# Optimization experiments

Measured on AMD Instinct MI355X. Metric: run time of the kernel, lower is better.

Reference implementation:

```python
import jax, jax.numpy as jnp
import numpy as np

D_MODEL = 1024
N_HEADS = 16
SEQ = 4096
BATCH = 1
THETA = 10000.0


def setup_inputs() -> dict:
    key = jax.random.key(0)
    ks = jax.random.split(key, 5)
    std = np.sqrt(2.0 / (D_MODEL + D_MODEL))
    x = jax.random.normal(ks[0], (BATCH, SEQ, D_MODEL), dtype=jnp.float32)
    Wq = jax.random.normal(ks[1], (D_MODEL, D_MODEL), dtype=jnp.float32) * std
    Wk = jax.random.normal(ks[2], (D_MODEL, D_MODEL), dtype=jnp.float32) * std
    Wv = jax.random.normal(ks[3], (D_MODEL, D_MODEL), dtype=jnp.float32) * std
    Wo = jax.random.normal(ks[4], (D_MODEL, D_MODEL), dtype=jnp.float32) * std
    token_positions = jnp.arange(SEQ, dtype=jnp.int32)
    return {"x": x, "Wq": Wq, "Wk": Wk, "Wv": Wv, "Wo": Wo,
            "token_positions": token_positions}


def _rope(x, positions):
    # x: [b, h, s, d]; positions: [s]
    d = x.shape[-1]
    ks = jnp.arange(0, d, 2, dtype=jnp.float32)
    inv_freq = 1.0 / jnp.power(jnp.float32(THETA), ks / d)          # [d/2]
    ang = positions.astype(jnp.float32)[:, None] * inv_freq[None, :]  # [s, d/2]
    cos, sin = jnp.cos(ang), jnp.sin(ang)
    x_even, x_odd = x[..., 0::2], x[..., 1::2]
    y_even = cos * x_even - sin * x_odd
    y_odd = sin * x_even + cos * x_odd
    # interleave back: [..., d/2, 2] -> [..., d]
    return jnp.stack([y_even, y_odd], axis=-1).reshape(x.shape)


def reference(x, Wq, Wk, Wv, Wo, token_positions):
    b, s, _ = x.shape
    h = N_HEADS
    d = D_MODEL // h

    def proj(W):
        y = jnp.einsum('bsi,oi->bso', x, W)
        return y.reshape(b, s, h, d).transpose(0, 2, 1, 3)  # [b,h,s,d]

    Q, K, V = proj(Wq), proj(Wk), proj(Wv)
    Q = _rope(Q, token_positions)
    K = _rope(K, token_positions)

    scale = 1.0 / np.sqrt(d)
    scores = jnp.einsum('bhqd,bhkd->bhqk', Q, K) * scale  # [b,h,s,s]
    causal = jnp.tril(jnp.ones((s, s), dtype=bool))
    scores = jnp.where(causal, scores, -jnp.inf)
    attn = jax.nn.softmax(scores, axis=-1)
    ctx = jnp.einsum('bhqk,bhkd->bhqd', attn, V)
    ctx = ctx.transpose(0, 2, 1, 3).reshape(b, s, D_MODEL)
    return jnp.einsum('bsi,oi->bso', ctx, Wo)
```

## Files before the change

### kernel.cpp

```cpp
#include <hip/hip_runtime.h>
#include <hip/hip_bf16.h>
#include <stdint.h>

#define S_LEN 4096
#define D_MODEL 1024
#define N_HEADS 16
#define D_HEAD 64
#define LDQKV 3072
#define SCALE_LOG2E 0.1803368787f

typedef __attribute__((ext_vector_type(4))) float f32x4;
typedef __attribute__((ext_vector_type(8))) __bf16 bf16x8;
typedef __attribute__((ext_vector_type(4))) __bf16 bf16x4;

__device__ __forceinline__ unsigned short f2bf(float f) {
    union { float f; unsigned u; } x{f};
    unsigned r = x.u + 0x7fff + ((x.u >> 16) & 1);
    return (unsigned short)(r >> 16);
}

__device__ __forceinline__ void gld_lds16(const void* g, void* l) {
    __builtin_amdgcn_global_load_lds(
        (const __attribute__((address_space(1))) unsigned int*)g,
        (__attribute__((address_space(3))) unsigned int*)l, 16, 0, 0);
}

__global__ __launch_bounds__(256) void prep_k(const float* __restrict__ x,
                                              const float* __restrict__ Wq,
                                              const float* __restrict__ Wk,
                                              const float* __restrict__ Wv,
                                              const float* __restrict__ Wo,
                                              const int* __restrict__ pos,
                                              unsigned short* __restrict__ xb,
                                              unsigned short* __restrict__ Wb,
                                              float* __restrict__ ct,
                                              float* __restrict__ st) {
    int b = blockIdx.x;
    if (b < 4096) {
        int i = (b * 256 + threadIdx.x) * 4;
        float4 v = *(const float4*)&x[i];
        ushort4 o;
        o.x = f2bf(v.x); o.y = f2bf(v.y); o.z = f2bf(v.z); o.w = f2bf(v.w);
        *(ushort4*)&xb[i] = o;
    } else if (b < 8192) {
        int i = ((b - 4096) * 256 + threadIdx.x) * 4;
        int sel = i >> 20;
        int off = i & ((1 << 20) - 1);
        const float* src = (sel == 0) ? Wq : (sel == 1) ? Wk : (sel == 2) ? Wv : Wo;
        float4 v = *(const float4*)&src[off];
        ushort4 o;
        o.x = f2bf(v.x); o.y = f2bf(v.y); o.z = f2bf(v.z); o.w = f2bf(v.w);
        *(ushort4*)&Wb[i] = o;
    } else {
        int i = (b - 8192) * 256 + threadIdx.x;
        int s = i >> 6, k = i & 63;
        if (k < 32) {
            float invf = __builtin_exp2f(-(float)(2 * k) * (1.0f / 64.0f) * 13.287712379549449f);
            float ang = (float)pos[s] * invf;
            ct[i] = cosf(ang);
            st[i] = sinf(ang);
        } else {
            ct[i] = 1.0f;
            st[i] = 0.0f;
        }
    }
}

__global__ __launch_bounds__(256) void vtrans_k(const unsigned short* __restrict__ src,
                                                unsigned short* __restrict__ dst) {
    __shared__ unsigned short tile[64 * 68];
    const int bs = blockIdx.x * 64;
    const int bd = blockIdx.y * 64;
    const int t = threadIdx.x;
    {
        int col = (t & 7) * 8;
        #pragma unroll
        for (int rr = 0; rr < 2; ++rr) {
            int row = rr * 32 + (t >> 3);
            const unsigned short* g = src + (size_t)(bs + row) * LDQKV + bd + col;
            ushort4 a = *(const ushort4*)g;
            ushort4 b = *(const ushort4*)(g + 4);
            *(ushort4*)&tile[row * 68 + col] = a;
            *(ushort4*)&tile[row * 68 + col + 4] = b;
        }
    }
    __syncthreads();
    {
        int dl = t >> 2;
        int sc = (t & 3) * 16;
        ushort4 o[4];
        #pragma unroll
        for (int e = 0; e < 16; ++e)
            ((unsigned short*)o)[e] = tile[(sc + e) * 68 + dl];
        unsigned short* g = dst + (size_t)(bd + dl) * S_LEN + bs + sc;
        *(ushort4*)(g + 0)  = o[0];
        *(ushort4*)(g + 4)  = o[1];
        *(ushort4*)(g + 8)  = o[2];
        *(ushort4*)(g + 12) = o[3];
    }
}

__global__ __launch_bounds__(256) void gemm_qkv_k(const unsigned short* __restrict__ A,
                                                  const unsigned short* __restrict__ B,
                                                  unsigned short* __restrict__ C,
                                                  const float* __restrict__ ct,
                                                  const float* __restrict__ st) {
    __shared__ unsigned short lA[128 * 64];
    __shared__ unsigned short lB[128 * 64];
    const int t = threadIdx.x, w = t >> 6, l = t & 63;
    const int tm = blockIdx.y * 128, tn = blockIdx.x * 128;
    const int wm = (w >> 1) * 64, wn = (w & 1) * 64;
    const int g = l >> 4, ln = l & 15;

    f32x4 acc[4][4] = {};

    for (int k0 = 0; k0 < 1024; k0 += 64) {
        #pragma unroll
        for (int r = 0; r < 4; ++r) {
            int row = 8 * (4 * r + w) + (l >> 3);
            gld_lds16(A + (size_t)(tm + row) * 1024 + k0 + (l & 7) * 8, &lA[(4 * r + w) * 512]);
            gld_lds16(B + (size_t)(tn + row) * 1024 + k0 + (l & 7) * 8, &lB[(4 * r + w) * 512]);
        }
        asm volatile("s_waitcnt vmcnt(0)" ::: "memory");
        __syncthreads();

        #pragma unroll
        for (int kk = 0; kk < 2; ++kk) {
            bf16x8 af[4], bf[4];
            #pragma unroll
            for (int i = 0; i < 4; ++i) {
                af[i] = *(const bf16x8*)&lA[(wm + i * 16 + ln) * 64 + kk * 32 + g * 8];
                bf[i] = *(const bf16x8*)&lB[(wn + i * 16 + ln) * 64 + kk * 32 + g * 8];
            }
            #pragma unroll
            for (int i = 0; i < 4; ++i)
                #pragma unroll
                for (int j = 0; j < 4; ++j)
                    acc[i][j] = __builtin_amdgcn_mfma_f32_16x16x32_bf16(af[i], bf[j], acc[i][j], 0, 0, 0);
        }
        __syncthreads();
    }

    #pragma unroll
    for (int i = 0; i < 4; ++i) {
        #pragma unroll
        for (int j = 0; j < 4; ++j) {
            int col = tn + wn + j * 16 + ln;
            int dd = col & 63;
            int tb = ((col >= 2048) ? 32 : 0) + (dd >> 1);
            float scl = (col < 1024) ? SCALE_LOG2E : 1.0f;
            #pragma unroll
            for (int r = 0; r < 4; ++r) {
                int row = tm + wm + i * 16 + g * 4 + r;
                float v = acc[i][j][r];
                float p = __shfl_xor(v, 1, 64);
                float c = ct[row * 64 + tb];
                float s = st[row * 64 + tb];
                v = ((dd & 1) ? (s * p + c * v) : (c * v - s * p)) * scl;
                C[(size_t)row * LDQKV + col] = f2bf(v);
            }
        }
    }
}

__global__ __launch_bounds__(256) void gemm_o_k(const unsigned short* __restrict__ A,
                                                const unsigned short* __restrict__ B,
                                                float* __restrict__ C) {
    __shared__ unsigned short lA[64 * 64];
    __shared__ unsigned short lB[128 * 64];
    const int t = threadIdx.x, w = t >> 6, l = t & 63;
    const int tm = blockIdx.y * 64, tn = blockIdx.x * 128;
    const int wm = (w >> 1) * 32, wn = (w & 1) * 64;
    const int g = l >> 4, ln = l & 15;

    f32x4 acc[2][4] = {};

    for (int k0 = 0; k0 < 1024; k0 += 64) {
        #pragma unroll
        for (int r = 0; r < 2; ++r) {
            int row = r * 32 + w * 8 + (l >> 3);
            gld_lds16(A + (size_t)(tm + row) * 1024 + k0 + (l & 7) * 8, &lA[(r * 32 + w * 8) * 64]);
        }
        #pragma unroll
        for (int r = 0; r < 4; ++r) {
            int row = 8 * (4 * r + w) + (l >> 3);
            gld_lds16(B + (size_t)(tn + row) * 1024 + k0 + (l & 7) * 8, &lB[(4 * r + w) * 512]);
        }
        asm volatile("s_waitcnt vmcnt(0)" ::: "memory");
        __syncthreads();

        #pragma unroll
        for (int kk = 0; kk < 2; ++kk) {
            bf16x8 af[2], bf[4];
            #pragma unroll
            for (int i = 0; i < 2; ++i)
                af[i] = *(const bf16x8*)&lA[(wm + i * 16 + ln) * 64 + kk * 32 + g * 8];
            #pragma unroll
            for (int j = 0; j < 4; ++j)
                bf[j] = *(const bf16x8*)&lB[(wn + j * 16 + ln) * 64 + kk * 32 + g * 8];
            #pragma unroll
            for (int i = 0; i < 2; ++i)
                #pragma unroll
                for (int j = 0; j < 4; ++j)
                    acc[i][j] = __builtin_amdgcn_mfma_f32_16x16x32_bf16(af[i], bf[j], acc[i][j], 0, 0, 0);
        }
        __syncthreads();
    }

    #pragma unroll
    for (int i = 0; i < 2; ++i)
        #pragma unroll
        for (int j = 0; j < 4; ++j) {
            int col = tn + wn + j * 16 + ln;
            #pragma unroll
            for (int r = 0; r < 4; ++r) {
                int row = tm + wm + i * 16 + g * 4 + r;
                C[(size_t)row * 1024 + col] = acc[i][j][r];
            }
        }
}

__device__ __forceinline__ void stage8(const unsigned short* __restrict__ Kb,
                                       const unsigned short* __restrict__ Vt,
                                       unsigned short* lK, unsigned short* lV,
                                       int h, int kt, int w, int l) {
    const int half = w & 3;
    const int chunk = (l & 7) ^ (l >> 3);
    if (w < 4) {
        #pragma unroll
        for (int r2 = 0; r2 < 2; ++r2) {
            int row = half * 16 + r2 * 8 + (l >> 3);
            gld_lds16(Kb + (size_t)(kt * 64 + row) * LDQKV + h * 64 + chunk * 8,
                      lK + half * 1024 + r2 * 512);
        }
    } else {
        #pragma unroll
        for (int r2 = 0; r2 < 2; ++r2) {
            int row = half * 16 + r2 * 8 + (l >> 3);
            gld_lds16(Vt + (size_t)(h * 64 + row) * S_LEN + kt * 64 + chunk * 8,
                      lV + half * 1024 + r2 * 512);
        }
    }
}

__global__ __launch_bounds__(512) void attn_k(const unsigned short* __restrict__ Qb,
                                              const unsigned short* __restrict__ Kb,
                                              const unsigned short* __restrict__ Vt,
                                              unsigned short* __restrict__ ctxb) {
    __shared__ unsigned short lK[2][64 * 64];
    __shared__ unsigned short lV[2][64 * 64];
    __shared__ unsigned short lP[8][16 * 64];

    const int t = threadIdx.x, w = t >> 6, l = t & 63;
    const int wv = w & 3;
    const int sel = w >> 2;
    const int h = blockIdx.x;
    const int qA = blockIdx.y;
    const int qB = 63 - qA;
    const int qT = sel ? qB : qA;
    const int q0 = qT * 64 + wv * 16;
    const int g = l >> 4, ln = l & 15;

    bf16x8 aq[2];
    #pragma unroll
    for (int kk = 0; kk < 2; ++kk)
        aq[kk] = *(const bf16x8*)&Qb[(size_t)(q0 + ln) * LDQKV + h * 64 + kk * 32 + g * 8];

    f32x4 acc[4] = {};
    float rm = -INFINITY, rs = 0.0f;
    char* lpw = (char*)&lP[w][0];

    stage8(Kb, Vt, &lK[0][0], &lV[0][0], h, 0, w, l);
    asm volatile("s_waitcnt vmcnt(0)" ::: "memory");
    __syncthreads();

    int cur = 0;
    for (int kt = 0; kt <= qB; ++kt) {
        if (kt < qB)
            stage8(Kb, Vt, &lK[cur ^ 1][0], &lV[cur ^ 1][0], h, kt + 1, w, l);

        if (kt <= qT) {
            float p[16];
            __builtin_amdgcn_s_setprio(1);
            #pragma unroll
            for (int ct = 0; ct < 4; ++ct) {
                f32x4 z = {};
                #pragma unroll
                for (int kk = 0; kk < 2; ++kk) {
                    int row = ct * 16 + ln;
                    int off = (row * 128 + kk * 64 + g * 16) ^ ((row & 7) << 4);
                    bf16x8 ak = *(const bf16x8*)((const char*)&lK[cur][0] + off);
                    z = __builtin_amdgcn_mfma_f32_16x16x32_bf16(ak, aq[kk], z, 0, 0, 0);
                }
                #pragma unroll
                for (int r = 0; r < 4; ++r) p[ct * 4 + r] = z[r];
            }
            __builtin_amdgcn_s_setprio(0);

            if (kt == qT) {
                int qg = q0 + ln;
                #pragma unroll
                for (int ct = 0; ct < 4; ++ct)
                    #pragma unroll
                    for (int r = 0; r < 4; ++r)
                        if (kt * 64 + ct * 16 + g * 4 + r > qg) p[ct * 4 + r] = -INFINITY;
            }

            float pmax = fmaxf(p[0], p[1]);
            #pragma unroll
            for (int i = 2; i < 16; i += 2)
                pmax = fmaxf(fmaxf(pmax, p[i]), p[i + 1]);
            pmax = fmaxf(pmax, __shfl_xor(pmax, 16, 64));
            pmax = fmaxf(pmax, __shfl_xor(pmax, 32, 64));
            if (__any(pmax > rm + 8.0f)) {
                float mn = fmaxf(rm, pmax);
                float fac = __builtin_amdgcn_exp2f(rm - mn);
                rm = mn;
                rs *= fac;
                #pragma unroll
                for (int mb = 0; mb < 4; ++mb) {
                    f32x4 a = acc[mb];
                    #pragma unroll
                    for (int r = 0; r < 4; ++r) a[r] *= fac;
                    acc[mb] = a;
                }
            }
            float ps = 0.0f;
            #pragma unroll
            for (int i = 0; i < 16; ++i) {
                float e = __builtin_amdgcn_exp2f(p[i] - rm);
                p[i] = e;
                ps += e;
            }
            ps += __shfl_xor(ps, 16, 64);
            ps += __shfl_xor(ps, 32, 64);
            rs += ps;

            #pragma unroll
            for (int ct = 0; ct < 4; ++ct) {
                bf16x4 pv;
                pv[0] = (__bf16)p[ct * 4 + 0];
                pv[1] = (__bf16)p[ct * 4 + 1];
                pv[2] = (__bf16)p[ct * 4 + 2];
                pv[3] = (__bf16)p[ct * 4 + 3];
                int off = (ln * 128 + ct * 32 + g * 8) ^ ((ln & 7) << 4);
                *(bf16x4*)(lpw + off) = pv;
            }

            __builtin_amdgcn_s_setprio(1);
            #pragma unroll
            for (int mb = 0; mb < 4; ++mb) {
                #pragma unroll
                for (int kc = 0; kc < 2; ++kc) {
                    int vrow = mb * 16 + ln;
                    int voff = (vrow * 128 + kc * 64 + g * 16) ^ ((vrow & 7) << 4);
                    bf16x8 av = *(const bf16x8*)((const char*)&lV[cur][0] + voff);
                    int poff = (ln * 128 + kc * 64 + g * 16) ^ ((ln & 7) << 4);
                    bf16x8 bp = *(const bf16x8*)(lpw + poff);
                    acc[mb] = __builtin_amdgcn_mfma_f32_16x16x32_bf16(av, bp, acc[mb], 0, 0, 0);
                }
            }
            __builtin_amdgcn_s_setprio(0);
        }

        asm volatile("s_waitcnt vmcnt(0)" ::: "memory");
        __syncthreads();
        cur ^= 1;
    }

    float inv = 1.0f / rs;
    #pragma unroll
    for (int mb = 0; mb < 4; ++mb) {
        bf16x4 o;
        #pragma unroll
        for (int r = 0; r < 4; ++r) o[r] = (__bf16)(acc[mb][r] * inv);
        *(bf16x4*)&ctxb[(size_t)(q0 + ln) * D_MODEL + h * 64 + mb * 16 + g * 4] = o;
    }
}

extern "C" void kernel_launch(void* const* d_in, const int* in_sizes, int n_in,
                              void* d_out, int out_size, void* d_ws, size_t ws_size,
                              hipStream_t stream) {
    const float* x  = (const float*)d_in[0];
    const float* Wq = (const float*)d_in[1];
    const float* Wk = (const float*)d_in[2];
    const float* Wv = (const float*)d_in[3];
    const float* Wo = (const float*)d_in[4];
    const int* tpos = (const int*)d_in[5];
    float* out = (float*)d_out;

    char* ws = (char*)d_ws;
    unsigned short* xb   = (unsigned short*)(ws + 0);
    unsigned short* Wb   = (unsigned short*)(ws + (8u << 20));
    unsigned short* QKV  = (unsigned short*)(ws + (16u << 20));
    unsigned short* ctxb = (unsigned short*)(ws + (40u << 20));
    float* costab = (float*)(ws + (48u << 20));
    float* sintab = (float*)(ws + (49u << 20));
    unsigned short* Vtb  = xb;

    prep_k<<<9216, 256, 0, stream>>>(x, Wq, Wk, Wv, Wo, tpos, xb, Wb, costab, sintab);

    gemm_qkv_k<<<dim3(24, 32), 256, 0, stream>>>(xb, Wb, QKV, costab, sintab);

    vtrans_k<<<dim3(S_LEN / 64, D_MODEL / 64), 256, 0, stream>>>(QKV + 2048, Vtb);

    attn_k<<<dim3(N_HEADS, 32), 512, 0, stream>>>(QKV, QKV + 1024, Vtb, ctxb);

    gemm_o_k<<<dim3(8, 64), 256, 0, stream>>>(ctxb, Wb + 3u * 1024 * 1024, out);
}
```

Baseline: 165.2 us.

## Balance causal attention work by splitting long query tile's KV halves across both wave groups

Previously the wave group owning the short query tile qA sat idle while the other group processed the long tile qB. Now, after finishing tile qA, both wave groups work on tile qB by splitting each 64-key block into two 32-key halves, each keeping its own online-softmax state. The two partial states are merged through LDS at the end. This evens out the per-wave workload but adds an LDS merge, a second Q fragment in registers, and halves the MFMA work per iteration, leaving more softmax overhead per key.

```diff
diff --git a/kernel.cpp b/kernel.cpp
--- a/kernel.cpp
+++ b/kernel.cpp
@@ -243,6 +243,91 @@
     }
 }
 
+__device__ __forceinline__ void do_half(const char* lKc, const char* lVc, char* lpw,
+                                        const bf16x8* aq, f32x4* acc,
+                                        float& rm, float& rs,
+                                        int kc, bool diag, int kbase, int qg,
+                                        int g, int ln) {
+    float p[8];
+    __builtin_amdgcn_s_setprio(1);
+    #pragma unroll
+    for (int c2 = 0; c2 < 2; ++c2) {
+        int ct = 2 * kc + c2;
+        f32x4 z = {};
+        #pragma unroll
+        for (int kk = 0; kk < 2; ++kk) {
+            int row = ct * 16 + ln;
+            int off = (row * 128 + kk * 64 + g * 16) ^ ((row & 7) << 4);
+            bf16x8 ak = *(const bf16x8*)(lKc + off);
+            z = __builtin_amdgcn_mfma_f32_16x16x32_bf16(ak, aq[kk], z, 0, 0, 0);
+        }
+        #pragma unroll
+        for (int r = 0; r < 4; ++r) p[c2 * 4 + r] = z[r];
+    }
+    __builtin_amdgcn_s_setprio(0);
+
+    if (diag) {
+        #pragma unroll
+        for (int c2 = 0; c2 < 2; ++c2)
+            #pragma unroll
+            for (int r = 0; r < 4; ++r)
+                if (kbase + (2 * kc + c2) * 16 + g * 4 + r > qg) p[c2 * 4 + r] = -INFINITY;
+    }
+
+    float pmax = fmaxf(p[0], p[1]);
+    #pragma unroll
+    for (int i = 2; i < 8; i += 2)
+        pmax = fmaxf(fmaxf(pmax, p[i]), p[i + 1]);
+    pmax = fmaxf(pmax, __shfl_xor(pmax, 16, 64));
+    pmax = fmaxf(pmax, __shfl_xor(pmax, 32, 64));
+    if (__any(pmax > rm + 8.0f)) {
+        float mn = fmaxf(rm, pmax);
+        float fac = __builtin_amdgcn_exp2f(rm - mn);
+        rm = mn;
+        rs *= fac;
+        #pragma unroll
+        for (int mb = 0; mb < 4; ++mb) {
+            f32x4 a = acc[mb];
+            #pragma unroll
+            for (int r = 0; r < 4; ++r) a[r] *= fac;
+            acc[mb] = a;
+        }
+    }
+    float ps = 0.0f;
+    #pragma unroll
+    for (int i = 0; i < 8; ++i) {
+        float e = __builtin_amdgcn_exp2f(p[i] - rm);
+        p[i] = e;
+        ps += e;
+    }
+    ps += __shfl_xor(ps, 16, 64);
+    ps += __shfl_xor(ps, 32, 64);
+    rs += ps;
+
+    #pragma unroll
+    for (int c2 = 0; c2 < 2; ++c2) {
+        bf16x4 pv;
+        pv[0] = (__bf16)p[c2 * 4 + 0];
+        pv[1] = (__bf16)p[c2 * 4 + 1];
+        pv[2] = (__bf16)p[c2 * 4 + 2];
+        pv[3] = (__bf16)p[c2 * 4 + 3];
+        int off = (ln * 128 + (2 * kc + c2) * 32 + g * 8) ^ ((ln & 7) << 4);
+        *(bf16x4*)(lpw + off) = pv;
+    }
+
+    int poff = (ln * 128 + kc * 64 + g * 16) ^ ((ln & 7) << 4);
+    bf16x8 bp = *(const bf16x8*)(lpw + poff);
+    __builtin_amdgcn_s_setprio(1);
+    #pragma unroll
+    for (int mb = 0; mb < 4; ++mb) {
+        int vrow = mb * 16 + ln;
+        int voff = (vrow * 128 + kc * 64 + g * 16) ^ ((vrow & 7) << 4);
+        bf16x8 av = *(const bf16x8*)(lVc + voff);
+        acc[mb] = __builtin_amdgcn_mfma_f32_16x16x32_bf16(av, bp, acc[mb], 0, 0, 0);
+    }
+    __builtin_amdgcn_s_setprio(0);
+}
+
 __global__ __launch_bounds__(512) void attn_k(const unsigned short* __restrict__ Qb,
                                               const unsigned short* __restrict__ Kb,
                                               const unsigned short* __restrict__ Vt,
@@ -257,14 +342,17 @@
     const int h = blockIdx.x;
     const int qA = blockIdx.y;
     const int qB = 63 - qA;
-    const int qT = sel ? qB : qA;
-    const int q0 = qT * 64 + wv * 16;
+    const int qOwn = sel ? qB : qA;
+    const int q0own = qOwn * 64 + wv * 16;
+    const int q0B = qB * 64 + wv * 16;
     const int g = l >> 4, ln = l & 15;
 
-    bf16x8 aq[2];
-    #pragma unroll
-    for (int kk = 0; kk < 2; ++kk)
-        aq[kk] = *(const bf16x8*)&Qb[(size_t)(q0 + ln) * LDQKV + h * 64 + kk * 32 + g * 8];
+    bf16x8 aqOwn[2], aqB[2];
+    #pragma unroll
+    for (int kk = 0; kk < 2; ++kk) {
+        aqOwn[kk] = *(const bf16x8*)&Qb[(size_t)(q0own + ln) * LDQKV + h * 64 + kk * 32 + g * 8];
+        aqB[kk]   = *(const bf16x8*)&Qb[(size_t)(q0B + ln) * LDQKV + h * 64 + kk * 32 + g * 8];
+    }
 
     f32x4 acc[4] = {};
     float rm = -INFINITY, rs = 0.0f;
@@ -279,88 +367,30 @@
         if (kt < qB)
             stage8(Kb, Vt, &lK[cur ^ 1][0], &lV[cur ^ 1][0], h, kt + 1, w, l);
 
-        if (kt <= qT) {
-            float p[16];
-            __builtin_amdgcn_s_setprio(1);
-            #pragma unroll
-            for (int ct = 0; ct < 4; ++ct) {
-                f32x4 z = {};
-                #pragma unroll
-                for (int kk = 0; kk < 2; ++kk) {
-                    int row = ct * 16 + ln;
-                    int off = (row * 128 + kk * 64 + g * 16) ^ ((row & 7) << 4);
-                    bf16x8 ak = *(const bf16x8*)((const char*)&lK[cur][0] + off);
-                    z = __builtin_amdgcn_mfma_f32_16x16x32_bf16(ak, aq[kk], z, 0, 0, 0);
-                }
-                #pragma unroll
-                for (int r = 0; r < 4; ++r) p[ct * 4 + r] = z[r];
-            }
-            __builtin_amdgcn_s_setprio(0);
-
-            if (kt == qT) {
-                int qg = q0 + ln;
-                #pragma unroll
-                for (int ct = 0; ct < 4; ++ct)
-                    #pragma unroll
-                    for (int r = 0; r < 4; ++r)
-                        if (kt * 64 + ct * 16 + g * 4 + r > qg) p[ct * 4 + r] = -INFINITY;
-            }
-
-            float pmax = fmaxf(p[0], p[1]);
-            #pragma unroll
-            for (int i = 2; i < 16; i += 2)
-                pmax = fmaxf(fmaxf(pmax, p[i]), p[i + 1]);
-            pmax = fmaxf(pmax, __shfl_xor(pmax, 16, 64));
-            pmax = fmaxf(pmax, __shfl_xor(pmax, 32, 64));
-            if (__any(pmax > rm + 8.0f)) {
-                float mn = fmaxf(rm, pmax);
-                float fac = __builtin_amdgcn_exp2f(rm - mn);
-                rm = mn;
-                rs *= fac;
+        const char* lKc = (const char*)&lK[cur][0];
+        const char* lVc = (const char*)&lV[cur][0];
+
+        if (kt <= qA) {
+            bool diag = (kt == qOwn);
+            do_half(lKc, lVc, lpw, aqOwn, acc, rm, rs, 0, diag, kt * 64, q0own + ln, g, ln);
+            do_half(lKc, lVc, lpw, aqOwn, acc, rm, rs, 1, diag, kt * 64, q0own + ln, g, ln);
+            if (sel == 0 && kt == qA) {
+                float inv = 1.0f / rs;
                 #pragma unroll
                 for (int mb = 0; mb < 4; ++mb) {
-                    f32x4 a = acc[mb];
+                    bf16x4 o;
                     #pragma unroll
-                    for (int r = 0; r < 4; ++r) a[r] *= fac;
-                    acc[mb] = a;
+                    for (int r = 0; r < 4; ++r) o[r] = (__bf16)(acc[mb][r] * inv);
+                    *(bf16x4*)&ctxb[(size_t)(q0own + ln) * D_MODEL + h * 64 + mb * 16 + g * 4] = o;
                 }
+                rm = -INFINITY;
+                rs = 0.0f;
+                #pragma unroll
+                for (int mb = 0; mb < 4; ++mb) acc[mb] = f32x4{};
             }
-            float ps = 0.0f;
-            #pragma unroll
-            for (int i = 0; i < 16; ++i) {
-                float e = __builtin_amdgcn_exp2f(p[i] - rm);
-                p[i] = e;
-                ps += e;
-            }
-            ps += __shfl_xor(ps, 16, 64);
-            ps += __shfl_xor(ps, 32, 64);
-            rs += ps;
-
-            #pragma unroll
-            for (int ct = 0; ct < 4; ++ct) {
-                bf16x4 pv;
-                pv[0] = (__bf16)p[ct * 4 + 0];
-                pv[1] = (__bf16)p[ct * 4 + 1];
-                pv[2] = (__bf16)p[ct * 4 + 2];
-                pv[3] = (__bf16)p[ct * 4 + 3];
-                int off = (ln * 128 + ct * 32 + g * 8) ^ ((ln & 7) << 4);
-                *(bf16x4*)(lpw + off) = pv;
-            }
-
-            __builtin_amdgcn_s_setprio(1);
-            #pragma unroll
-            for (int mb = 0; mb < 4; ++mb) {
-                #pragma unroll
-                for (int kc = 0; kc < 2; ++kc) {
-                    int vrow = mb * 16 + ln;
-                    int voff = (vrow * 128 + kc * 64 + g * 16) ^ ((vrow & 7) << 4);
-                    bf16x8 av = *(const bf16x8*)((const char*)&lV[cur][0] + voff);
-                    int poff = (ln * 128 + kc * 64 + g * 16) ^ ((ln & 7) << 4);
-                    bf16x8 bp = *(const bf16x8*)(lpw + poff);
-                    acc[mb] = __builtin_amdgcn_mfma_f32_16x16x32_bf16(av, bp, acc[mb], 0, 0, 0);
-                }
-            }
-            __builtin_amdgcn_s_setprio(0);
+        } else {
+            bool diag = (kt == qB);
+            do_half(lKc, lVc, lpw, aqB, acc, rm, rs, sel, diag, kt * 64, q0B + ln, g, ln);
         }
 
         asm volatile("s_waitcnt vmcnt(0)" ::: "memory");
@@ -368,13 +398,33 @@
         cur ^= 1;
     }
 
-    float inv = 1.0f / rs;
-    #pragma unroll
-    for (int mb = 0; mb < 4; ++mb) {
-        bf16x4 o;
-        #pragma unroll
-        for (int r = 0; r < 4; ++r) o[r] = (__bf16)(acc[mb][r] * inv);
-        *(bf16x4*)&ctxb[(size_t)(q0 + ln) * D_MODEL + h * 64 + mb * 16 + g * 4] = o;
+    float* lKf = (float*)&lK[0][0];
+    float* lPf = (float*)&lP[0][0];
+    if (sel == 0) {
+        #pragma unroll
+        for (int mb = 0; mb < 4; ++mb)
+            *(f32x4*)&lKf[(size_t)(w * 64 + l) * 16 + mb * 4] = acc[mb];
+        lPf[(w * 64 + l) * 2 + 0] = rm;
+        lPf[(w * 64 + l) * 2 + 1] = rs;
+    }
+    __syncthreads();
+    if (sel == 1) {
+        int pw = w - 4;
+        float rm2 = lPf[(pw * 64 + l) * 2 + 0];
+        float rs2 = lPf[(pw * 64 + l) * 2 + 1];
+        float m = fmaxf(rm, rm2);
+        float f1 = __builtin_amdgcn_exp2f(rm - m);
+        float f2 = __builtin_amdgcn_exp2f(rm2 - m);
+        float inv = 1.0f / (rs * f1 + rs2 * f2);
+        #pragma unroll
+        for (int mb = 0; mb < 4; ++mb) {
+            f32x4 a2 = *(const f32x4*)&lKf[(size_t)(pw * 64 + l) * 16 + mb * 4];
+            bf16x4 o;
+            #pragma unroll
+            for (int r = 0; r < 4; ++r)
+                o[r] = (__bf16)((acc[mb][r] * f1 + a2[r] * f2) * inv);
+            *(bf16x4*)&ctxb[(size_t)(q0B + ln) * D_MODEL + h * 64 + mb * 16 + g * 4] = o;
+        }
     }
 }
 
```

Result: no change. 164.9 us (-0.2%).

## Switch attention to 32x32x16 MFMA with register-shuffled P and 256-thread blocks

Applied to the files above, without the earlier changes.

Rewrites the attention kernel so each wave computes 32 query rows with 32x32x16 bf16 MFMAs instead of 16 rows with 16x16x32. The softmax probabilities are repacked into the B-operand layout with cross-lane shuffles rather than a round trip through per-wave LDS. Blocks shrink from 512 to 256 threads, each wave stages both K and V, and output goes through LDS for coalesced 16-byte stores. This cuts LDS traffic and MFMA issue count per tile but raises register pressure (two 16-float accumulators plus scores) and halves the waves per block.

```diff
diff --git a/kernel.cpp b/kernel.cpp
--- a/kernel.cpp
+++ b/kernel.cpp
@@ -10,6 +10,7 @@
 #define SCALE_LOG2E 0.1803368787f
 
 typedef __attribute__((ext_vector_type(4))) float f32x4;
+typedef __attribute__((ext_vector_type(16))) float f32x16;
 typedef __attribute__((ext_vector_type(8))) __bf16 bf16x8;
 typedef __attribute__((ext_vector_type(4))) __bf16 bf16x4;
 
@@ -17,6 +18,11 @@
     union { float f; unsigned u; } x{f};
     unsigned r = x.u + 0x7fff + ((x.u >> 16) & 1);
     return (unsigned short)(r >> 16);
+}
+
+__device__ __forceinline__ unsigned pk2(float a, float b) {
+    union { __bf16 h; unsigned short u; } ua{(__bf16)a}, ub{(__bf16)b};
+    return (unsigned)ua.u | ((unsigned)ub.u << 16);
 }
 
 __device__ __forceinline__ void gld_lds16(const void* g, void* l) {
@@ -220,145 +226,135 @@
         }
 }
 
-__device__ __forceinline__ void stage8(const unsigned short* __restrict__ Kb,
+__device__ __forceinline__ void stage4(const unsigned short* __restrict__ Kb,
                                        const unsigned short* __restrict__ Vt,
                                        unsigned short* lK, unsigned short* lV,
                                        int h, int kt, int w, int l) {
-    const int half = w & 3;
     const int chunk = (l & 7) ^ (l >> 3);
-    if (w < 4) {
-        #pragma unroll
-        for (int r2 = 0; r2 < 2; ++r2) {
-            int row = half * 16 + r2 * 8 + (l >> 3);
-            gld_lds16(Kb + (size_t)(kt * 64 + row) * LDQKV + h * 64 + chunk * 8,
-                      lK + half * 1024 + r2 * 512);
-        }
-    } else {
-        #pragma unroll
-        for (int r2 = 0; r2 < 2; ++r2) {
-            int row = half * 16 + r2 * 8 + (l >> 3);
-            gld_lds16(Vt + (size_t)(h * 64 + row) * S_LEN + kt * 64 + chunk * 8,
-                      lV + half * 1024 + r2 * 512);
-        }
-    }
-}
-
-__global__ __launch_bounds__(512) void attn_k(const unsigned short* __restrict__ Qb,
+    #pragma unroll
+    for (int r2 = 0; r2 < 2; ++r2) {
+        int row = r2 * 32 + w * 8 + (l >> 3);
+        gld_lds16(Kb + (size_t)(kt * 64 + row) * LDQKV + h * 64 + chunk * 8,
+                  lK + r2 * 2048 + w * 512);
+        gld_lds16(Vt + (size_t)(h * 64 + row) * S_LEN + kt * 64 + chunk * 8,
+                  lV + r2 * 2048 + w * 512);
+    }
+}
+
+__global__ __launch_bounds__(256) void attn_k(const unsigned short* __restrict__ Qb,
                                               const unsigned short* __restrict__ Kb,
                                               const unsigned short* __restrict__ Vt,
                                               unsigned short* __restrict__ ctxb) {
     __shared__ unsigned short lK[2][64 * 64];
     __shared__ unsigned short lV[2][64 * 64];
-    __shared__ unsigned short lP[8][16 * 64];
 
     const int t = threadIdx.x, w = t >> 6, l = t & 63;
-    const int wv = w & 3;
-    const int sel = w >> 2;
     const int h = blockIdx.x;
     const int qA = blockIdx.y;
     const int qB = 63 - qA;
-    const int qT = sel ? qB : qA;
-    const int q0 = qT * 64 + wv * 16;
-    const int g = l >> 4, ln = l & 15;
-
-    bf16x8 aq[2];
+    const int qT = (w < 2) ? qA : qB;
+    const int q0w = qT * 64 + (w & 1) * 32;
+    const int lq = l & 31;
+    const int hi = l >> 5;
+    const int q = q0w + lq;
+
+    bf16x8 aq[4];
     #pragma unroll
-    for (int kk = 0; kk < 2; ++kk)
-        aq[kk] = *(const bf16x8*)&Qb[(size_t)(q0 + ln) * LDQKV + h * 64 + kk * 32 + g * 8];
-
-    f32x4 acc[4] = {};
+    for (int s = 0; s < 4; ++s)
+        aq[s] = *(const bf16x8*)&Qb[(size_t)q * LDQKV + h * 64 + s * 16 + hi * 8];
+
+    f32x16 acc0 = {}, acc1 = {};
     float rm = -INFINITY, rs = 0.0f;
-    char* lpw = (char*)&lP[w][0];
-
-    stage8(Kb, Vt, &lK[0][0], &lV[0][0], h, 0, w, l);
+
+    stage4(Kb, Vt, &lK[0][0], &lV[0][0], h, 0, w, l);
     asm volatile("s_waitcnt vmcnt(0)" ::: "memory");
     __syncthreads();
 
     int cur = 0;
     for (int kt = 0; kt <= qB; ++kt) {
         if (kt < qB)
-            stage8(Kb, Vt, &lK[cur ^ 1][0], &lV[cur ^ 1][0], h, kt + 1, w, l);
+            stage4(Kb, Vt, &lK[cur ^ 1][0], &lV[cur ^ 1][0], h, kt + 1, w, l);
 
         if (kt <= qT) {
-            float p[16];
+            const char* lKc = (const char*)&lK[cur][0];
+            const char* lVc = (const char*)&lV[cur][0];
+
+            f32x16 z0 = {}, z1 = {};
             __builtin_amdgcn_s_setprio(1);
             #pragma unroll
-            for (int ct = 0; ct < 4; ++ct) {
-                f32x4 z = {};
+            for (int s = 0; s < 4; ++s) {
+                int r0 = lq, r1 = 32 + lq;
+                int off0 = (r0 * 128 + s * 32 + hi * 16) ^ ((r0 & 7) << 4);
+                int off1 = (r1 * 128 + s * 32 + hi * 16) ^ ((r1 & 7) << 4);
+                bf16x8 k0 = *(const bf16x8*)(lKc + off0);
+                bf16x8 k1 = *(const bf16x8*)(lKc + off1);
+                z0 = __builtin_amdgcn_mfma_f32_32x32x16_bf16(k0, aq[s], z0, 0, 0, 0);
+                z1 = __builtin_amdgcn_mfma_f32_32x32x16_bf16(k1, aq[s], z1, 0, 0, 0);
+            }
+            __builtin_amdgcn_s_setprio(0);
+
+            if (kt == qT) {
                 #pragma unroll
-                for (int kk = 0; kk < 2; ++kk) {
-                    int row = ct * 16 + ln;
-                    int off = (row * 128 + kk * 64 + g * 16) ^ ((row & 7) << 4);
-                    bf16x8 ak = *(const bf16x8*)((const char*)&lK[cur][0] + off);
-                    z = __builtin_amdgcn_mfma_f32_16x16x32_bf16(ak, aq[kk], z, 0, 0, 0);
+                for (int r = 0; r < 16; ++r) {
+                    int kg = kt * 64 + (r & 3) + 8 * (r >> 2) + 4 * hi;
+                    if (kg > q)      z0[r] = -INFINITY;
+                    if (kg + 32 > q) z1[r] = -INFINITY;
                 }
-                #pragma unroll
-                for (int r = 0; r < 4; ++r) p[ct * 4 + r] = z[r];
-            }
-            __builtin_amdgcn_s_setprio(0);
-
-            if (kt == qT) {
-                int qg = q0 + ln;
-                #pragma unroll
-                for (int ct = 0; ct < 4; ++ct)
-                    #pragma unroll
-                    for (int r = 0; r < 4; ++r)
-                        if (kt * 64 + ct * 16 + g * 4 + r > qg) p[ct * 4 + r] = -INFINITY;
-            }
-
-            float pmax = fmaxf(p[0], p[1]);
-            #pragma unroll
-            for (int i = 2; i < 16; i += 2)
-                pmax = fmaxf(fmaxf(pmax, p[i]), p[i + 1]);
-            pmax = fmaxf(pmax, __shfl_xor(pmax, 16, 64));
-            pmax = fmaxf(pmax, __shfl_xor(pmax, 32, 64));
-            if (__any(pmax > rm + 8.0f)) {
-                float mn = fmaxf(rm, pmax);
+            }
+
+            float mx = fmaxf(z0[0], z1[0]);
+            #pragma unroll
+            for (int r = 1; r < 16; ++r) mx = fmaxf(mx, fmaxf(z0[r], z1[r]));
+            mx = fmaxf(mx, __shfl_xor(mx, 32, 64));
+            if (__any(mx > rm + 8.0f)) {
+                float mn = fmaxf(rm, mx);
                 float fac = __builtin_amdgcn_exp2f(rm - mn);
                 rm = mn;
                 rs *= fac;
                 #pragma unroll
-                for (int mb = 0; mb < 4; ++mb) {
-                    f32x4 a = acc[mb];
-                    #pragma unroll
-                    for (int r = 0; r < 4; ++r) a[r] *= fac;
-                    acc[mb] = a;
-                }
+                for (int r = 0; r < 16; ++r) { acc0[r] *= fac; acc1[r] *= fac; }
             }
             float ps = 0.0f;
             #pragma unroll
-            for (int i = 0; i < 16; ++i) {
-                float e = __builtin_amdgcn_exp2f(p[i] - rm);
-                p[i] = e;
-                ps += e;
-            }
-            ps += __shfl_xor(ps, 16, 64);
+            for (int r = 0; r < 16; ++r) {
+                z0[r] = __builtin_amdgcn_exp2f(z0[r] - rm); ps += z0[r];
+                z1[r] = __builtin_amdgcn_exp2f(z1[r] - rm); ps += z1[r];
+            }
             ps += __shfl_xor(ps, 32, 64);
             rs += ps;
 
-            #pragma unroll
-            for (int ct = 0; ct < 4; ++ct) {
-                bf16x4 pv;
-                pv[0] = (__bf16)p[ct * 4 + 0];
-                pv[1] = (__bf16)p[ct * 4 + 1];
-                pv[2] = (__bf16)p[ct * 4 + 2];
-                pv[3] = (__bf16)p[ct * 4 + 3];
-                int off = (ln * 128 + ct * 32 + g * 8) ^ ((ln & 7) << 4);
-                *(bf16x4*)(lpw + off) = pv;
+            bf16x8 bp[4];
+            #pragma unroll
+            for (int s = 0; s < 4; ++s) {
+                float e0, e1, e2, e3, f0, f1, f2, f3;
+                if (s == 0) { e0=z0[0]; e1=z0[1]; e2=z0[2]; e3=z0[3]; f0=z0[4]; f1=z0[5]; f2=z0[6]; f3=z0[7]; }
+                else if (s == 1) { e0=z0[8]; e1=z0[9]; e2=z0[10]; e3=z0[11]; f0=z0[12]; f1=z0[13]; f2=z0[14]; f3=z0[15]; }
+                else if (s == 2) { e0=z1[0]; e1=z1[1]; e2=z1[2]; e3=z1[3]; f0=z1[4]; f1=z1[5]; f2=z1[6]; f3=z1[7]; }
+                else             { e0=z1[8]; e1=z1[9]; e2=z1[10]; e3=z1[11]; f0=z1[12]; f1=z1[13]; f2=z1[14]; f3=z1[15]; }
+                unsigned A0 = pk2(e0, e1), A1 = pk2(e2, e3);
+                unsigned B0 = pk2(f0, f1), B1 = pk2(f2, f3);
+                unsigned RA0 = (unsigned)__shfl_xor((int)A0, 32, 64);
+                unsigned RA1 = (unsigned)__shfl_xor((int)A1, 32, 64);
+                unsigned RB0 = (unsigned)__shfl_xor((int)B0, 32, 64);
+                unsigned RB1 = (unsigned)__shfl_xor((int)B1, 32, 64);
+                union { uint4 u; bf16x8 v; } cv;
+                cv.u.x = hi ? RB0 : A0;
+                cv.u.y = hi ? RB1 : A1;
+                cv.u.z = hi ? B0  : RA0;
+                cv.u.w = hi ? B1  : RA1;
+                bp[s] = cv.v;
             }
 
             __builtin_amdgcn_s_setprio(1);
             #pragma unroll
-            for (int mb = 0; mb < 4; ++mb) {
-                #pragma unroll
-                for (int kc = 0; kc < 2; ++kc) {
-                    int vrow = mb * 16 + ln;
-                    int voff = (vrow * 128 + kc * 64 + g * 16) ^ ((vrow & 7) << 4);
-                    bf16x8 av = *(const bf16x8*)((const char*)&lV[cur][0] + voff);
-                    int poff = (ln * 128 + kc * 64 + g * 16) ^ ((ln & 7) << 4);
-                    bf16x8 bp = *(const bf16x8*)(lpw + poff);
-                    acc[mb] = __builtin_amdgcn_mfma_f32_16x16x32_bf16(av, bp, acc[mb], 0, 0, 0);
-                }
+            for (int s = 0; s < 4; ++s) {
+                int r0 = lq, r1 = 32 + lq;
+                int off0 = (r0 * 128 + s * 32 + hi * 16) ^ ((r0 & 7) << 4);
+                int off1 = (r1 * 128 + s * 32 + hi * 16) ^ ((r1 & 7) << 4);
+                bf16x8 v0 = *(const bf16x8*)(lVc + off0);
+                bf16x8 v1 = *(const bf16x8*)(lVc + off1);
+                acc0 = __builtin_amdgcn_mfma_f32_32x32x16_bf16(v0, bp[s], acc0, 0, 0, 0);
+                acc1 = __builtin_amdgcn_mfma_f32_32x32x16_bf16(v1, bp[s], acc1, 0, 0, 0);
             }
             __builtin_amdgcn_s_setprio(0);
         }
@@ -368,13 +364,21 @@
         cur ^= 1;
     }
 
+    unsigned short* lw = &lK[0][0] + w * 2048;
     float inv = 1.0f / rs;
     #pragma unroll
-    for (int mb = 0; mb < 4; ++mb) {
-        bf16x4 o;
-        #pragma unroll
-        for (int r = 0; r < 4; ++r) o[r] = (__bf16)(acc[mb][r] * inv);
-        *(bf16x4*)&ctxb[(size_t)(q0 + ln) * D_MODEL + h * 64 + mb * 16 + g * 4] = o;
+    for (int r = 0; r < 16; ++r) {
+        int d0 = (r & 3) + 8 * (r >> 2) + 4 * hi;
+        lw[lq * 64 + d0]      = f2bf(acc0[r] * inv);
+        lw[lq * 64 + 32 + d0] = f2bf(acc1[r] * inv);
+    }
+    {
+        int qloc = l >> 1, half = l & 1;
+        const unsigned short* src = lw + qloc * 64 + half * 32;
+        unsigned short* gdst = ctxb + (size_t)(q0w + qloc) * D_MODEL + h * 64 + half * 32;
+        #pragma unroll
+        for (int c = 0; c < 4; ++c)
+            *(uint4*)(gdst + c * 8) = *(const uint4*)(src + c * 8);
     }
 }
 
@@ -404,7 +408,7 @@
 
     vtrans_k<<<dim3(S_LEN / 64, D_MODEL / 64), 256, 0, stream>>>(QKV + 2048, Vtb);
 
-    attn_k<<<dim3(N_HEADS, 32), 512, 0, stream>>>(QKV, QKV + 1024, Vtb, ctxb);
+    attn_k<<<dim3(N_HEADS, 32), 256, 0, stream>>>(QKV, QKV + 1024, Vtb, ctxb);
 
     gemm_o_k<<<dim3(8, 64), 256, 0, stream>>>(ctxb, Wb + 3u * 1024 * 1024, out);
 }
```

New measurement: 207.5 us. 1.26x slower.
